# Optimization experiments

Hardware: AMD Instinct MI355X
Metric: run time of the kernel (lower is better)

## Reference

```python
import jax, jax.numpy as jnp
import numpy as np

B, N, CIN, K = 4, 4096, 64, 16
MLP = [64, 64, 128]
EPS = 1e-5


def setup_inputs() -> dict:
    key = jax.random.key(0)
    ks = jax.random.split(key, 8)
    inp = {
        "xyz": jax.random.normal(ks[0], (B, N, 3), dtype=jnp.float32),
        "points": jax.random.normal(ks[1], (B, N, CIN), dtype=jnp.float32),
    }
    last = 3 + CIN
    for i, oc in enumerate(MLP):
        inp[f"w{i}"] = jax.random.normal(ks[2 + i], (oc, last), dtype=jnp.float32) * 0.05
        inp[f"b{i}"] = jnp.zeros((oc,), dtype=jnp.float32)
        inp[f"g{i}"] = jnp.ones((oc,), dtype=jnp.float32)
        inp[f"be{i}"] = jnp.zeros((oc,), dtype=jnp.float32)
        inp[f"rm{i}"] = jnp.zeros((oc,), dtype=jnp.float32)
        inp[f"rv{i}"] = jnp.ones((oc,), dtype=jnp.float32)
        last = oc
    return inp


def reference(xyz, points, w0, b0, g0, be0, rm0, rv0,
              w1, b1, g1, be1, rm1, rv1,
              w2, b2, g2, be2, rm2, rv2):
    # knn via squared pairwise distance (same argsort order as cdist)
    sq = jnp.sum(xyz * xyz, axis=-1)  # (B,N)
    d2 = sq[:, :, None] + sq[:, None, :] - 2.0 * jnp.einsum('bnc,bmc->bnm', xyz, xyz)
    _, idx = jax.lax.top_k(-d2, K)  # (B,N,K), smallest-distance neighbors

    bidx = jnp.arange(xyz.shape[0])[:, None, None]  # (B,1,1)
    grouped_xyz = xyz[bidx, idx] - xyz[:, :, None, :]     # (B,N,K,3) relative coords
    grouped_pts = points[bidx, idx]                        # (B,N,K,CIN)
    h = jnp.concatenate([grouped_xyz, grouped_pts], axis=-1)  # (B,N,K,3+CIN)

    layers = [(w0, b0, g0, be0, rm0, rv0),
              (w1, b1, g1, be1, rm1, rv1),
              (w2, b2, g2, be2, rm2, rv2)]
    for (w, b, g, be, rm, rv) in layers:
        # 1x1 conv == per-point linear; BN in eval mode (running stats)
        h = jnp.einsum('bnkc,oc->bnko', h, w) + b
        h = (h - rm) * jax.lax.rsqrt(rv + EPS) * g + be
        h = jax.nn.relu(h)
    new_points = jnp.max(h, axis=2)  # max over K neighbors -> (B,N,C_out)
    return new_points
```

## Files before the change

### kernel.cpp

```cpp
#include <hip/hip_runtime.h>

#define NPT   4096
#define KNN_K 16
#define EPSV  1e-5f

#define W0T_OFF 0
#define B0_OFF  4288
#define W1T_OFF 4352
#define B1_OFF  8448
#define W2T_OFF 8512
#define B2_OFF  16704
#define IDX_OFF 16832
#define XYZ4_OFF 278976
#define P_OFF   344512
#define Q_OFF   1393088

typedef unsigned long long ull;

__global__ void prep_kernel(
    const float* __restrict__ xyz,
    const float* __restrict__ w0, const float* __restrict__ b0, const float* __restrict__ g0,
    const float* __restrict__ be0, const float* __restrict__ rm0, const float* __restrict__ rv0,
    const float* __restrict__ w1, const float* __restrict__ b1, const float* __restrict__ g1,
    const float* __restrict__ be1, const float* __restrict__ rm1, const float* __restrict__ rv1,
    const float* __restrict__ w2, const float* __restrict__ b2, const float* __restrict__ g2,
    const float* __restrict__ be2, const float* __restrict__ rm2, const float* __restrict__ rv2,
    float* __restrict__ ws) {
  int blk = blockIdx.x;
  if (blk < 64) {
    int i = blk * 256 + threadIdx.x;
    const float* p = xyz + i * 3;
    float x = p[0], y = p[1], z = p[2];
    float sq = __fadd_rn(__fadd_rn(__fmul_rn(x, x), __fmul_rn(y, y)), __fmul_rn(z, z));
    ((float4*)(ws + XYZ4_OFF))[i] = make_float4(x, y, z, sq);
    return;
  }
  int i = (blk - 64) * 256 + threadIdx.x;
  if (i < 4288) {
    int oc = i & 63, icp = i >> 6;
    int col = (icp < 64) ? (icp + 3) : (icp - 64);
    float s = g0[oc] * rsqrtf(rv0[oc] + EPSV);
    ws[W0T_OFF + i] = w0[oc * 67 + col] * s;
  } else if (i < 4352) {
    int oc = i - 4288;
    float s = g0[oc] * rsqrtf(rv0[oc] + EPSV);
    ws[i] = (b0[oc] - rm0[oc]) * s + be0[oc];
  } else if (i < 8448) {
    int j = i - 4352; int oc = j & 63, ic = j >> 6;
    float s = g1[oc] * rsqrtf(rv1[oc] + EPSV);
    ws[i] = w1[oc * 64 + ic] * s;
  } else if (i < 8512) {
    int oc = i - 8448;
    float s = g1[oc] * rsqrtf(rv1[oc] + EPSV);
    ws[i] = (b1[oc] - rm1[oc]) * s + be1[oc];
  } else if (i < 16704) {
    int j = i - 8512; int ic = j >> 7, oc = j & 127;
    float s = g2[oc] * rsqrtf(rv2[oc] + EPSV);
    ws[i] = w2[oc * 64 + ic] * s;
  } else if (i < 16832) {
    int oc = i - 16704;
    float s = g2[oc] * rsqrtf(rv2[oc] + EPSV);
    ws[i] = (b2[oc] - rm2[oc]) * s + be2[oc];
  }
}

__global__ __launch_bounds__(256) void pq_kernel(const float* __restrict__ xyz,
                                                 const float* __restrict__ points,
                                                 float* __restrict__ ws) {
  int tid = threadIdx.x;
  int oc = tid & 63;
  int i = blockIdx.x * 4 + (tid >> 6);
  const float* w0t = ws + W0T_OFF;
  float x = xyz[i * 3], y = xyz[i * 3 + 1], z = xyz[i * 3 + 2];
  float qacc = w0t[64 * 64 + oc] * x;
  qacc = fmaf(w0t[65 * 64 + oc], y, qacc);
  qacc = fmaf(w0t[66 * 64 + oc], z, qacc);
  float acc = ws[B0_OFF + oc] + qacc;
  const float* prow = points + (size_t)i * 64;
#pragma unroll 4
  for (int c = 0; c < 64; ++c) acc = fmaf(w0t[c * 64 + oc], prow[c], acc);
  ws[P_OFF + (size_t)i * 64 + oc] = acc;
  ws[Q_OFF + (size_t)i * 64 + oc] = qacc;
}

__device__ __forceinline__ ull minu64(ull a, ull b) { return a < b ? a : b; }
__device__ __forceinline__ ull maxu64(ull a, ull b) { return a > b ? a : b; }

__device__ __forceinline__ ull bitonic_sort64(ull v, int lane) {
#pragma unroll
  for (int k = 2; k <= 64; k <<= 1) {
#pragma unroll
    for (int j = k >> 1; j > 0; j >>= 1) {
      ull o = __shfl_xor(v, j);
      bool lower = (lane & j) == 0;
      bool up = (lane & k) == 0;
      v = (lower == up) ? minu64(v, o) : maxu64(v, o);
    }
  }
  return v;
}

__device__ __forceinline__ ull bitonic_merge64(ull v, int lane) {
#pragma unroll
  for (int j = 32; j > 0; j >>= 1) {
    ull o = __shfl_xor(v, j);
    v = ((lane & j) == 0) ? minu64(v, o) : maxu64(v, o);
  }
  return v;
}

__global__ __launch_bounds__(256) void knn_kernel(const float4* __restrict__ cand4,
                                                  int* __restrict__ knnOut) {
  __shared__ __align__(16) float4 tile[1024];
  __shared__ ull buf[4][128];
  int tid = threadIdx.x;
  int lane = tid & 63, w = tid >> 6;
  int b = blockIdx.x >> 10;
  int n = ((blockIdx.x & 1023) << 2) + w;
  const float4* cb = cand4 + b * NPT;

  float4 q = cb[n];
  ull R = ~0ull;
  ull thresh = ~0ull;
  int cnt = 0;
  ull ltmask = (lane == 0) ? 0ull : (~0ull >> (64 - lane));

#pragma unroll 1
  for (int t = 0; t < 4; ++t) {
    __syncthreads();
#pragma unroll
    for (int j = 0; j < 4; ++j) tile[j * 256 + tid] = cb[t * 1024 + j * 256 + tid];
    __syncthreads();
#pragma unroll 1
    for (int i = 0; i < 16; ++i) {
      int ml = (i << 6) + lane;
      float4 c = tile[ml];
      float dot = __fadd_rn(__fadd_rn(__fmul_rn(q.x, c.x), __fmul_rn(q.y, c.y)),
                            __fmul_rn(q.z, c.z));
      float d2 = __fsub_rn(__fadd_rn(q.w, c.w), __fmul_rn(2.0f, dot));
      unsigned bits = __float_as_uint(d2);
      unsigned fk = bits ^ (0x80000000u | (unsigned)((int)bits >> 31));
      ull key = ((ull)fk << 32) | (unsigned)((t << 10) + ml);
      bool pred = key < thresh;
      ull mask = __ballot(pred);
      if (mask) {
        int pos = cnt + __popcll(mask & ltmask);
        if (pred) buf[w][pos] = key;
        cnt += __popcll(mask);
        if (cnt >= 64) {
          ull v = buf[w][lane];
          v = bitonic_sort64(v, lane);
          ull vr = __shfl(v, 63 - lane);
          R = minu64(R, vr);
          R = bitonic_merge64(R, lane);
          thresh = __shfl(R, 15);
          cnt -= 64;
          if (lane < cnt) {
            ull tmp = buf[w][64 + lane];
            buf[w][lane] = tmp;
          }
        }
      }
    }
  }
  {
    ull v = (lane < cnt) ? buf[w][lane] : ~0ull;
    v = bitonic_sort64(v, lane);
    ull vr = __shfl(v, 63 - lane);
    R = minu64(R, vr);
    R = bitonic_merge64(R, lane);
  }
  if (lane < KNN_K)
    knnOut[(b * NPT + n) * KNN_K + lane] = (int)(unsigned)(R & 0xFFFFFFFFull);
}

__global__ __launch_bounds__(256) void mlp_kernel(
    const float* __restrict__ wbuf, const int* __restrict__ knn,
    float* __restrict__ out) {
  __shared__ __align__(16) float Ash[64 * 128];
  __shared__ __align__(16) float Wsh[64 * 64];
  int tid = threadIdx.x;
  int qblk = blockIdx.x << 3;

  const float4* w1g = (const float4*)(wbuf + W1T_OFF);
  float4 st0 = w1g[tid];
  float4 st1 = w1g[256 + tid];
  float4 st2 = w1g[512 + tid];
  float4 st3 = w1g[768 + tid];

  {
    int p = tid & 127, half = tid >> 7;
    int q = qblk + (p >> 4);
    int k = p & 15;
    int src = knn[q * KNN_K + k];
    int srow = (q & ~(NPT - 1)) + src;
    const float4* Pp = (const float4*)(wbuf + P_OFF + (size_t)srow * 64 + half * 32);
    const float4* Qp = (const float4*)(wbuf + Q_OFF + (size_t)q * 64 + half * 32);
#pragma unroll
    for (int j = 0; j < 8; ++j) {
      float4 pv = Pp[j];
      float4 qv = Qp[j];
      int ic = half * 32 + j * 4;
      Ash[(ic + 0) * 128 + p] = fmaxf(pv.x - qv.x, 0.0f);
      Ash[(ic + 1) * 128 + p] = fmaxf(pv.y - qv.y, 0.0f);
      Ash[(ic + 2) * 128 + p] = fmaxf(pv.z - qv.z, 0.0f);
      Ash[(ic + 3) * 128 + p] = fmaxf(pv.w - qv.w, 0.0f);
    }
  }
  {
    float4* wl = (float4*)Wsh;
    wl[tid] = st0; wl[256 + tid] = st1; wl[512 + tid] = st2; wl[768 + tid] = st3;
  }
  const float4* w2g = (const float4*)(wbuf + W2T_OFF);
  {
    int r0 = tid, r1 = 256 + tid, r2 = 512 + tid, r3 = 768 + tid;
    st0 = w2g[(r0 >> 4) * 32 + (r0 & 15)];
    st1 = w2g[(r1 >> 4) * 32 + (r1 & 15)];
    st2 = w2g[(r2 >> 4) * 32 + (r2 & 15)];
    st3 = w2g[(r3 >> 4) * 32 + (r3 & 15)];
  }
  __syncthreads();

  int og = tid & 7, pg = tid >> 3;
  const float* Arow = Ash + 4 * pg;
  const float* Wrow = Wsh + 8 * og;
  float acc[4][8];

  {
    float4 b0v = *(const float4*)(wbuf + B1_OFF + 8 * og);
    float4 b1v = *(const float4*)(wbuf + B1_OFF + 8 * og + 4);
    float bj[8] = {b0v.x, b0v.y, b0v.z, b0v.w, b1v.x, b1v.y, b1v.z, b1v.w};
#pragma unroll
    for (int i = 0; i < 4; ++i)
#pragma unroll
      for (int j = 0; j < 8; ++j) acc[i][j] = bj[j];
#pragma unroll 4
    for (int ic = 0; ic < 64; ++ic) {
      float4 a0 = *(const float4*)(Arow + ic * 128);
      float4 w0 = *(const float4*)(Wrow + ic * 64);
      float4 w1v = *(const float4*)(Wrow + ic * 64 + 4);
      float av[4] = {a0.x, a0.y, a0.z, a0.w};
      float wv[8] = {w0.x, w0.y, w0.z, w0.w, w1v.x, w1v.y, w1v.z, w1v.w};
#pragma unroll
      for (int i = 0; i < 4; ++i)
#pragma unroll
        for (int j = 0; j < 8; ++j) acc[i][j] = fmaf(av[i], wv[j], acc[i][j]);
    }
  }
  __syncthreads();
#pragma unroll
  for (int j = 0; j < 8; ++j) {
    int oc = 8 * og + j;
    *(float4*)(Ash + oc * 128 + 4 * pg) =
        make_float4(fmaxf(acc[0][j], 0.0f), fmaxf(acc[1][j], 0.0f),
                    fmaxf(acc[2][j], 0.0f), fmaxf(acc[3][j], 0.0f));
  }
  {
    float4* wl = (float4*)Wsh;
    wl[tid] = st0; wl[256 + tid] = st1; wl[512 + tid] = st2; wl[768 + tid] = st3;
    int r0 = tid, r1 = 256 + tid, r2 = 512 + tid, r3 = 768 + tid;
    st0 = w2g[(r0 >> 4) * 32 + 16 + (r0 & 15)];
    st1 = w2g[(r1 >> 4) * 32 + 16 + (r1 & 15)];
    st2 = w2g[(r2 >> 4) * 32 + 16 + (r2 & 15)];
    st3 = w2g[(r3 >> 4) * 32 + 16 + (r3 & 15)];
  }
  __syncthreads();

  int qout = qblk + (pg >> 2);
  float* obase = out + (size_t)qout * 128 + 8 * og;
#pragma unroll 1
  for (int pass = 0; pass < 2; ++pass) {
    {
      float4 b0v = *(const float4*)(wbuf + B2_OFF + pass * 64 + 8 * og);
      float4 b1v = *(const float4*)(wbuf + B2_OFF + pass * 64 + 8 * og + 4);
      float bj[8] = {b0v.x, b0v.y, b0v.z, b0v.w, b1v.x, b1v.y, b1v.z, b1v.w};
#pragma unroll
      for (int i = 0; i < 4; ++i)
#pragma unroll
        for (int j = 0; j < 8; ++j) acc[i][j] = bj[j];
    }
#pragma unroll 4
    for (int ic = 0; ic < 64; ++ic) {
      float4 a0 = *(const float4*)(Arow + ic * 128);
      float4 w0 = *(const float4*)(Wrow + ic * 64);
      float4 w1v = *(const float4*)(Wrow + ic * 64 + 4);
      float av[4] = {a0.x, a0.y, a0.z, a0.w};
      float wv[8] = {w0.x, w0.y, w0.z, w0.w, w1v.x, w1v.y, w1v.z, w1v.w};
#pragma unroll
      for (int i = 0; i < 4; ++i)
#pragma unroll
        for (int j = 0; j < 8; ++j) acc[i][j] = fmaf(av[i], wv[j], acc[i][j]);
    }
    float m[8];
#pragma unroll
    for (int j = 0; j < 8; ++j) {
      float v = fmaxf(fmaxf(acc[0][j], acc[1][j]), fmaxf(acc[2][j], acc[3][j]));
      v = fmaxf(v, 0.0f);
      v = fmaxf(v, __shfl_xor(v, 8));
      m[j] = fmaxf(v, __shfl_xor(v, 16));
    }
    if ((pg & 3) == 0) {
      *(float4*)(obase + pass * 64)     = make_float4(m[0], m[1], m[2], m[3]);
      *(float4*)(obase + pass * 64 + 4) = make_float4(m[4], m[5], m[6], m[7]);
    }
    if (pass == 0) {
      __syncthreads();
      float4* wl = (float4*)Wsh;
      wl[tid] = st0; wl[256 + tid] = st1; wl[512 + tid] = st2; wl[768 + tid] = st3;
      __syncthreads();
    }
  }
}

extern "C" void kernel_launch(void* const* d_in, const int* in_sizes, int n_in,
                              void* d_out, int out_size, void* d_ws, size_t ws_size,
                              hipStream_t stream) {
  const float* xyz    = (const float*)d_in[0];
  const float* points = (const float*)d_in[1];
  float* wsF = (float*)d_ws;
  int* idxBuf = (int*)(wsF + IDX_OFF);
  const float4* cand4 = (const float4*)(wsF + XYZ4_OFF);

  prep_kernel<<<130, 256, 0, stream>>>(
      xyz,
      (const float*)d_in[2],  (const float*)d_in[3],  (const float*)d_in[4],
      (const float*)d_in[5],  (const float*)d_in[6],  (const float*)d_in[7],
      (const float*)d_in[8],  (const float*)d_in[9],  (const float*)d_in[10],
      (const float*)d_in[11], (const float*)d_in[12], (const float*)d_in[13],
      (const float*)d_in[14], (const float*)d_in[15], (const float*)d_in[16],
      (const float*)d_in[17], (const float*)d_in[18], (const float*)d_in[19],
      wsF);
  pq_kernel<<<4096, 256, 0, stream>>>(xyz, points, wsF);
  knn_kernel<<<4096, 256, 0, stream>>>(cand4, idxBuf);
  mlp_kernel<<<2048, 256, 0, stream>>>(wsF, idxBuf, (float*)d_out);
}
```

Measured before the change: 265.0 us.

## Merge prep, pq and knn kernels into one horizontally fused launch

```diff
diff --git a/kernel.cpp b/kernel.cpp
--- a/kernel.cpp
+++ b/kernel.cpp
@@ -4,174 +4,181 @@
 #define KNN_K 16
 #define EPSV  1e-5f
 
-#define W0T_OFF 0
-#define B0_OFF  4288
 #define W1T_OFF 4352
 #define B1_OFF  8448
 #define W2T_OFF 8512
 #define B2_OFF  16704
 #define IDX_OFF 16832
-#define XYZ4_OFF 278976
 #define P_OFF   344512
 #define Q_OFF   1393088
 
 typedef unsigned long long ull;
 
-__global__ void prep_kernel(
-    const float* __restrict__ xyz,
+__device__ __forceinline__ ull minu64(ull a, ull b) { return a < b ? a : b; }
+__device__ __forceinline__ ull maxu64(ull a, ull b) { return a > b ? a : b; }
+
+__device__ __forceinline__ ull bitonic_sort64(ull v, int lane) {
+#pragma unroll
+  for (int k = 2; k <= 64; k <<= 1) {
+#pragma unroll
+    for (int j = k >> 1; j > 0; j >>= 1) {
+      ull o = __shfl_xor(v, j);
+      bool lower = (lane & j) == 0;
+      bool up = (lane & k) == 0;
+      v = (lower == up) ? minu64(v, o) : maxu64(v, o);
+    }
+  }
+  return v;
+}
+
+__device__ __forceinline__ ull bitonic_merge64(ull v, int lane) {
+#pragma unroll
+  for (int j = 32; j > 0; j >>= 1) {
+    ull o = __shfl_xor(v, j);
+    v = ((lane & j) == 0) ? minu64(v, o) : maxu64(v, o);
+  }
+  return v;
+}
+
+__global__ __launch_bounds__(256) void mega_kernel(
+    const float* __restrict__ xyz, const float* __restrict__ points,
     const float* __restrict__ w0, const float* __restrict__ b0, const float* __restrict__ g0,
     const float* __restrict__ be0, const float* __restrict__ rm0, const float* __restrict__ rv0,
     const float* __restrict__ w1, const float* __restrict__ b1, const float* __restrict__ g1,
     const float* __restrict__ be1, const float* __restrict__ rm1, const float* __restrict__ rv1,
     const float* __restrict__ w2, const float* __restrict__ b2, const float* __restrict__ g2,
     const float* __restrict__ be2, const float* __restrict__ rm2, const float* __restrict__ rv2,
-    float* __restrict__ ws) {
+    float* __restrict__ ws, int* __restrict__ knnOut) {
+  __shared__ __align__(16) unsigned char smem[20480];
   int blk = blockIdx.x;
-  if (blk < 64) {
-    int i = blk * 256 + threadIdx.x;
-    const float* p = xyz + i * 3;
-    float x = p[0], y = p[1], z = p[2];
-    float sq = __fadd_rn(__fadd_rn(__fmul_rn(x, x), __fmul_rn(y, y)), __fmul_rn(z, z));
-    ((float4*)(ws + XYZ4_OFF))[i] = make_float4(x, y, z, sq);
-    return;
-  }
-  int i = (blk - 64) * 256 + threadIdx.x;
-  if (i < 4288) {
-    int oc = i & 63, icp = i >> 6;
-    int col = (icp < 64) ? (icp + 3) : (icp - 64);
-    float s = g0[oc] * rsqrtf(rv0[oc] + EPSV);
-    ws[W0T_OFF + i] = w0[oc * 67 + col] * s;
-  } else if (i < 4352) {
-    int oc = i - 4288;
-    float s = g0[oc] * rsqrtf(rv0[oc] + EPSV);
-    ws[i] = (b0[oc] - rm0[oc]) * s + be0[oc];
-  } else if (i < 8448) {
-    int j = i - 4352; int oc = j & 63, ic = j >> 6;
-    float s = g1[oc] * rsqrtf(rv1[oc] + EPSV);
-    ws[i] = w1[oc * 64 + ic] * s;
-  } else if (i < 8512) {
-    int oc = i - 8448;
-    float s = g1[oc] * rsqrtf(rv1[oc] + EPSV);
-    ws[i] = (b1[oc] - rm1[oc]) * s + be1[oc];
-  } else if (i < 16704) {
-    int j = i - 8512; int ic = j >> 7, oc = j & 127;
-    float s = g2[oc] * rsqrtf(rv2[oc] + EPSV);
-    ws[i] = w2[oc * 64 + ic] * s;
-  } else if (i < 16832) {
-    int oc = i - 16704;
-    float s = g2[oc] * rsqrtf(rv2[oc] + EPSV);
-    ws[i] = (b2[oc] - rm2[oc]) * s + be2[oc];
-  }
-}
-
-__global__ __launch_bounds__(256) void pq_kernel(const float* __restrict__ xyz,
-                                                 const float* __restrict__ points,
-                                                 float* __restrict__ ws) {
   int tid = threadIdx.x;
-  int oc = tid & 63;
-  int i = blockIdx.x * 4 + (tid >> 6);
-  const float* w0t = ws + W0T_OFF;
-  float x = xyz[i * 3], y = xyz[i * 3 + 1], z = xyz[i * 3 + 2];
-  float qacc = w0t[64 * 64 + oc] * x;
-  qacc = fmaf(w0t[65 * 64 + oc], y, qacc);
-  qacc = fmaf(w0t[66 * 64 + oc], z, qacc);
-  float acc = ws[B0_OFF + oc] + qacc;
-  const float* prow = points + (size_t)i * 64;
-#pragma unroll 4
-  for (int c = 0; c < 64; ++c) acc = fmaf(w0t[c * 64 + oc], prow[c], acc);
-  ws[P_OFF + (size_t)i * 64 + oc] = acc;
-  ws[Q_OFF + (size_t)i * 64 + oc] = qacc;
-}
-
-__device__ __forceinline__ ull minu64(ull a, ull b) { return a < b ? a : b; }
-__device__ __forceinline__ ull maxu64(ull a, ull b) { return a > b ? a : b; }
-
-__device__ __forceinline__ ull bitonic_sort64(ull v, int lane) {
-#pragma unroll
-  for (int k = 2; k <= 64; k <<= 1) {
-#pragma unroll
-    for (int j = k >> 1; j > 0; j >>= 1) {
-      ull o = __shfl_xor(v, j);
-      bool lower = (lane & j) == 0;
-      bool up = (lane & k) == 0;
-      v = (lower == up) ? minu64(v, o) : maxu64(v, o);
-    }
-  }
-  return v;
-}
-
-__device__ __forceinline__ ull bitonic_merge64(ull v, int lane) {
-#pragma unroll
-  for (int j = 32; j > 0; j >>= 1) {
-    ull o = __shfl_xor(v, j);
-    v = ((lane & j) == 0) ? minu64(v, o) : maxu64(v, o);
-  }
-  return v;
-}
-
-__global__ __launch_bounds__(256) void knn_kernel(const float4* __restrict__ cand4,
-                                                  int* __restrict__ knnOut) {
-  __shared__ __align__(16) float4 tile[1024];
-  __shared__ ull buf[4][128];
-  int tid = threadIdx.x;
-  int lane = tid & 63, w = tid >> 6;
-  int b = blockIdx.x >> 10;
-  int n = ((blockIdx.x & 1023) << 2) + w;
-  const float4* cb = cand4 + b * NPT;
-
-  float4 q = cb[n];
-  ull R = ~0ull;
-  ull thresh = ~0ull;
-  int cnt = 0;
-  ull ltmask = (lane == 0) ? 0ull : (~0ull >> (64 - lane));
+
+  if (blk < 4096) {
+    float4* tile = (float4*)smem;
+    ull* buf = (ull*)(smem + 16384);
+    int lane = tid & 63, w = tid >> 6;
+    int b = blk >> 10;
+    int n = ((blk & 1023) << 2) + w;
+    const float* xb = xyz + (size_t)b * NPT * 3;
+
+    float4 q;
+    {
+      const float* qp = xb + n * 3;
+      float qx = qp[0], qy = qp[1], qz = qp[2];
+      float qsq = __fadd_rn(__fadd_rn(__fmul_rn(qx, qx), __fmul_rn(qy, qy)),
+                            __fmul_rn(qz, qz));
+      q = make_float4(qx, qy, qz, qsq);
+    }
+    ull R = ~0ull;
+    ull thresh = ~0ull;
+    int cnt = 0;
+    ull ltmask = (lane == 0) ? 0ull : (~0ull >> (64 - lane));
+    const float4* r4 = (const float4*)xb;
 
 #pragma unroll 1
-  for (int t = 0; t < 4; ++t) {
-    __syncthreads();
-#pragma unroll
-    for (int j = 0; j < 4; ++j) tile[j * 256 + tid] = cb[t * 1024 + j * 256 + tid];
-    __syncthreads();
+    for (int t = 0; t < 4; ++t) {
+      __syncthreads();
+      {
+        int fo = 768 * t + 3 * tid;
+        float4 A = r4[fo], B = r4[fo + 1], C = r4[fo + 2];
+        float xs[4] = {A.x, A.w, B.z, C.y};
+        float ys[4] = {A.y, B.x, B.w, C.z};
+        float zs[4] = {A.z, B.y, C.x, C.w};
+#pragma unroll
+        for (int j = 0; j < 4; ++j) {
+          float sq = __fadd_rn(__fadd_rn(__fmul_rn(xs[j], xs[j]), __fmul_rn(ys[j], ys[j])),
+                               __fmul_rn(zs[j], zs[j]));
+          tile[4 * tid + j] = make_float4(xs[j], ys[j], zs[j], sq);
+        }
+      }
+      __syncthreads();
 #pragma unroll 1
-    for (int i = 0; i < 16; ++i) {
-      int ml = (i << 6) + lane;
-      float4 c = tile[ml];
-      float dot = __fadd_rn(__fadd_rn(__fmul_rn(q.x, c.x), __fmul_rn(q.y, c.y)),
-                            __fmul_rn(q.z, c.z));
-      float d2 = __fsub_rn(__fadd_rn(q.w, c.w), __fmul_rn(2.0f, dot));
-      unsigned bits = __float_as_uint(d2);
-      unsigned fk = bits ^ (0x80000000u | (unsigned)((int)bits >> 31));
-      ull key = ((ull)fk << 32) | (unsigned)((t << 10) + ml);
-      bool pred = key < thresh;
-      ull mask = __ballot(pred);
-      if (mask) {
-        int pos = cnt + __popcll(mask & ltmask);
-        if (pred) buf[w][pos] = key;
-        cnt += __popcll(mask);
-        if (cnt >= 64) {
-          ull v = buf[w][lane];
-          v = bitonic_sort64(v, lane);
-          ull vr = __shfl(v, 63 - lane);
-          R = minu64(R, vr);
-          R = bitonic_merge64(R, lane);
-          thresh = __shfl(R, 15);
-          cnt -= 64;
-          if (lane < cnt) {
-            ull tmp = buf[w][64 + lane];
-            buf[w][lane] = tmp;
+      for (int i = 0; i < 16; ++i) {
+        int ml = (i << 6) + lane;
+        float4 c = tile[ml];
+        float dot = __fadd_rn(__fadd_rn(__fmul_rn(q.x, c.x), __fmul_rn(q.y, c.y)),
+                              __fmul_rn(q.z, c.z));
+        float d2 = __fsub_rn(__fadd_rn(q.w, c.w), __fmul_rn(2.0f, dot));
+        unsigned bits = __float_as_uint(d2);
+        unsigned fk = bits ^ (0x80000000u | (unsigned)((int)bits >> 31));
+        ull key = ((ull)fk << 32) | (unsigned)((t << 10) + ml);
+        bool pred = key < thresh;
+        ull mask = __ballot(pred);
+        if (mask) {
+          int pos = cnt + __popcll(mask & ltmask);
+          if (pred) buf[w * 128 + pos] = key;
+          cnt += __popcll(mask);
+          if (cnt >= 64) {
+            ull v = buf[w * 128 + lane];
+            v = bitonic_sort64(v, lane);
+            ull vr = __shfl(v, 63 - lane);
+            R = minu64(R, vr);
+            R = bitonic_merge64(R, lane);
+            thresh = __shfl(R, 15);
+            cnt -= 64;
+            if (lane < cnt) {
+              ull tmp = buf[w * 128 + 64 + lane];
+              buf[w * 128 + lane] = tmp;
+            }
           }
         }
       }
     }
-  }
-  {
-    ull v = (lane < cnt) ? buf[w][lane] : ~0ull;
-    v = bitonic_sort64(v, lane);
-    ull vr = __shfl(v, 63 - lane);
-    R = minu64(R, vr);
-    R = bitonic_merge64(R, lane);
-  }
-  if (lane < KNN_K)
-    knnOut[(b * NPT + n) * KNN_K + lane] = (int)(unsigned)(R & 0xFFFFFFFFull);
+    {
+      ull v = (lane < cnt) ? buf[w * 128 + lane] : ~0ull;
+      v = bitonic_sort64(v, lane);
+      ull vr = __shfl(v, 63 - lane);
+      R = minu64(R, vr);
+      R = bitonic_merge64(R, lane);
+    }
+    if (lane < KNN_K)
+      knnOut[(b * NPT + n) * KNN_K + lane] = (int)(unsigned)(R & 0xFFFFFFFFull);
+    return;
+  }
+
+  if (blk < 8192) {
+    float* wlds = (float*)smem;
+    for (int j = tid; j < 4288; j += 256) wlds[j] = w0[j];
+    __syncthreads();
+    int oc = tid & 63;
+    int i = (blk - 4096) * 4 + (tid >> 6);
+    float s = g0[oc] * rsqrtf(rv0[oc] + EPSV);
+    float b0f = (b0[oc] - rm0[oc]) * s + be0[oc];
+    const float* wrow = wlds + oc * 67;
+    float x = xyz[i * 3], y = xyz[i * 3 + 1], z = xyz[i * 3 + 2];
+    float qacc = __fmul_rn(wrow[0], s) * x;
+    qacc = fmaf(__fmul_rn(wrow[1], s), y, qacc);
+    qacc = fmaf(__fmul_rn(wrow[2], s), z, qacc);
+    float acc = b0f + qacc;
+    const float* prow = points + (size_t)i * 64;
+#pragma unroll 4
+    for (int c = 0; c < 64; ++c)
+      acc = fmaf(__fmul_rn(wrow[3 + c], s), prow[c], acc);
+    ws[P_OFF + (size_t)i * 64 + oc] = acc;
+    ws[Q_OFF + (size_t)i * 64 + oc] = qacc;
+    return;
+  }
+
+  {
+    int i = (blk - 8192) * 256 + tid + 4352;
+    if (i < 8448) {
+      int j = i - 4352; int oc = j & 63, ic = j >> 6;
+      float s = g1[oc] * rsqrtf(rv1[oc] + EPSV);
+      ws[i] = w1[oc * 64 + ic] * s;
+    } else if (i < 8512) {
+      int oc = i - 8448;
+      float s = g1[oc] * rsqrtf(rv1[oc] + EPSV);
+      ws[i] = (b1[oc] - rm1[oc]) * s + be1[oc];
+    } else if (i < 16704) {
+      int j = i - 8512; int ic = j >> 7, oc = j & 127;
+      float s = g2[oc] * rsqrtf(rv2[oc] + EPSV);
+      ws[i] = w2[oc * 64 + ic] * s;
+    } else if (i < 16832) {
+      int oc = i - 16704;
+      float s = g2[oc] * rsqrtf(rv2[oc] + EPSV);
+      ws[i] = (b2[oc] - rm2[oc]) * s + be2[oc];
+    }
+  }
 }
 
 __global__ __launch_bounds__(256) void mlp_kernel(
@@ -234,13 +241,13 @@
     for (int i = 0; i < 4; ++i)
 #pragma unroll
       for (int j = 0; j < 8; ++j) acc[i][j] = bj[j];
-#pragma unroll 4
+#pragma unroll 8
     for (int ic = 0; ic < 64; ++ic) {
       float4 a0 = *(const float4*)(Arow + ic * 128);
-      float4 w0 = *(const float4*)(Wrow + ic * 64);
+      float4 w0v = *(const float4*)(Wrow + ic * 64);
       float4 w1v = *(const float4*)(Wrow + ic * 64 + 4);
       float av[4] = {a0.x, a0.y, a0.z, a0.w};
-      float wv[8] = {w0.x, w0.y, w0.z, w0.w, w1v.x, w1v.y, w1v.z, w1v.w};
+      float wv[8] = {w0v.x, w0v.y, w0v.z, w0v.w, w1v.x, w1v.y, w1v.z, w1v.w};
 #pragma unroll
       for (int i = 0; i < 4; ++i)
 #pragma unroll
@@ -279,13 +286,13 @@
 #pragma unroll
         for (int j = 0; j < 8; ++j) acc[i][j] = bj[j];
     }
-#pragma unroll 4
+#pragma unroll 8
     for (int ic = 0; ic < 64; ++ic) {
       float4 a0 = *(const float4*)(Arow + ic * 128);
-      float4 w0 = *(const float4*)(Wrow + ic * 64);
+      float4 w0v = *(const float4*)(Wrow + ic * 64);
       float4 w1v = *(const float4*)(Wrow + ic * 64 + 4);
       float av[4] = {a0.x, a0.y, a0.z, a0.w};
-      float wv[8] = {w0.x, w0.y, w0.z, w0.w, w1v.x, w1v.y, w1v.z, w1v.w};
+      float wv[8] = {w0v.x, w0v.y, w0v.z, w0v.w, w1v.x, w1v.y, w1v.z, w1v.w};
 #pragma unroll
       for (int i = 0; i < 4; ++i)
 #pragma unroll
@@ -319,18 +326,15 @@
   const float* points = (const float*)d_in[1];
   float* wsF = (float*)d_ws;
   int* idxBuf = (int*)(wsF + IDX_OFF);
-  const float4* cand4 = (const float4*)(wsF + XYZ4_OFF);
-
-  prep_kernel<<<130, 256, 0, stream>>>(
-      xyz,
+
+  mega_kernel<<<8241, 256, 0, stream>>>(
+      xyz, points,
       (const float*)d_in[2],  (const float*)d_in[3],  (const float*)d_in[4],
       (const float*)d_in[5],  (const float*)d_in[6],  (const float*)d_in[7],
       (const float*)d_in[8],  (const float*)d_in[9],  (const float*)d_in[10],
       (const float*)d_in[11], (const float*)d_in[12], (const float*)d_in[13],
       (const float*)d_in[14], (const float*)d_in[15], (const float*)d_in[16],
       (const float*)d_in[17], (const float*)d_in[18], (const float*)d_in[19],
-      wsF);
-  pq_kernel<<<4096, 256, 0, stream>>>(xyz, points, wsF);
-  knn_kernel<<<4096, 256, 0, stream>>>(cand4, idxBuf);
+      wsF, idxBuf);
   mlp_kernel<<<2048, 256, 0, stream>>>(wsF, idxBuf, (float*)d_out);
 }
```

New measurement: 266.0 us. Within noise of the previous version (+0.4%).
